# Kernel tuning notes

Hardware: AMD Instinct MI355X
Metric: run time of the kernel (lower is better)

The kernel has to match this reference:

```python
import jax, jax.numpy as jnp
import numpy as np

NQ, BS, NP_, D = 100, 8, 17, 256
NH, L, P = 8, 4, 4
DH = D // NH
DFF = 1024
SHAPES = [(92, 92), (46, 46), (23, 23), (12, 12)]
LEN_IN = sum(h * w for h, w in SHAPES)


def setup_inputs() -> dict:
    key = jax.random.key(0)
    ks = jax.random.split(key, 20)
    def nrm(k, shape, s=0.02):
        return jax.random.normal(k, shape, jnp.float32) * s
    return {
        "tgt_pose": jax.random.normal(ks[0], (NQ, BS, NP_, D), jnp.float32),
        "tgt_pose_query_pos": jax.random.normal(ks[1], (NQ, BS, NP_, D), jnp.float32),
        "tgt_pose_reference_points": jax.random.uniform(ks[2], (NQ, BS, NP_, L, 2), jnp.float32),
        "memory": jax.random.normal(ks[3], (BS, LEN_IN, D), jnp.float32),
        "w_in_w": nrm(ks[4], (3 * D, D)), "b_in_w": jnp.zeros((3 * D,), jnp.float32),
        "w_out_w": nrm(ks[5], (D, D)), "b_out_w": jnp.zeros((D,), jnp.float32),
        "w_in_a": nrm(ks[6], (3 * D, D)), "b_in_a": jnp.zeros((3 * D,), jnp.float32),
        "w_out_a": nrm(ks[7], (D, D)), "b_out_a": jnp.zeros((D,), jnp.float32),
        "w_off": nrm(ks[8], (NH * L * P * 2, D)), "b_off": nrm(ks[9], (NH * L * P * 2,), 0.1),
        "w_aw": nrm(ks[10], (NH * L * P, D)), "b_aw": jnp.zeros((NH * L * P,), jnp.float32),
        "w_val": nrm(ks[11], (D, D)), "b_val": jnp.zeros((D,), jnp.float32),
        "w_oc": nrm(ks[12], (D, D)), "b_oc": jnp.zeros((D,), jnp.float32),
        "g_w": jnp.ones((D,), jnp.float32), "be_w": jnp.zeros((D,), jnp.float32),
        "g_a": jnp.ones((D,), jnp.float32), "be_a": jnp.zeros((D,), jnp.float32),
        "g1": jnp.ones((D,), jnp.float32), "be1": jnp.zeros((D,), jnp.float32),
        "g2": jnp.ones((D,), jnp.float32), "be2": jnp.zeros((D,), jnp.float32),
        "w1": nrm(ks[13], (DFF, D)), "b1": jnp.zeros((DFF,), jnp.float32),
        "w2": nrm(ks[14], (D, DFF)), "b2": jnp.zeros((D,), jnp.float32),
        "memory_key_padding_mask": jnp.zeros((BS, LEN_IN), jnp.bool_),
        "memory_spatial_shapes": jnp.array(SHAPES, jnp.int32),
        "memory_level_start_index": jnp.array(np.cumsum([0] + [h * w for h, w in SHAPES[:-1]]), jnp.int32),
    }


def _ln(x, g, b, eps=1e-5):
    m = x.mean(-1, keepdims=True)
    v = ((x - m) ** 2).mean(-1, keepdims=True)
    return (x - m) * jax.lax.rsqrt(v + eps) * g + b


def _mha(q, k, v, w_in, b_in, w_out, b_out):
    # q,k,v: [B, S, D] batch-first; torch nn.MultiheadAttention math
    B, S, d = q.shape
    qp = (q @ w_in[:d].T + b_in[:d]).reshape(B, S, NH, DH)
    kp = (k @ w_in[d:2 * d].T + b_in[d:2 * d]).reshape(B, -1, NH, DH)
    vp = (v @ w_in[2 * d:].T + b_in[2 * d:]).reshape(B, -1, NH, DH)
    att = jax.nn.softmax(jnp.einsum('bqhd,bkhd->bhqk', qp, kp) / jnp.sqrt(jnp.float32(DH)), axis=-1)
    o = jnp.einsum('bhqk,bkhd->bqhd', att, vp).reshape(B, S, d)
    return o @ w_out.T + b_out


def _bilinear(v, loc, Hl, Wl):
    # v: [Hl*Wl, NH, DH]; loc: [Lq, NH, P, 2] normalized to [0,1]; grid_sample align_corners=False, zero pad
    x = loc[..., 0] * Wl - 0.5
    y = loc[..., 1] * Hl - 0.5
    x0 = jnp.floor(x); y0 = jnp.floor(y)
    wx = x - x0; wy = y - y0
    x0i = x0.astype(jnp.int32); y0i = y0.astype(jnp.int32)
    hid = jnp.arange(NH)[None, :, None]
    def tap(yi, xi, w):
        ok = (xi >= 0) & (xi < Wl) & (yi >= 0) & (yi < Hl)
        idx = jnp.clip(yi, 0, Hl - 1) * Wl + jnp.clip(xi, 0, Wl - 1)
        return jnp.where(ok[..., None], v[idx, hid], 0.0) * w[..., None]
    return (tap(y0i, x0i, (1 - wy) * (1 - wx)) + tap(y0i, x0i + 1, (1 - wy) * wx)
            + tap(y0i + 1, x0i, wy * (1 - wx)) + tap(y0i + 1, x0i + 1, wy * wx))


def _deform(query, ref, memory, mask, shapes, starts, w_off, b_off, w_aw, b_aw, w_val, b_val, w_oc, b_oc):
    # Multi-scale deformable attention (MSDeformAttn)
    bs, lq, d = query.shape
    value = memory @ w_val.T + b_val
    value = jnp.where(mask[..., None], 0.0, value).reshape(bs, -1, NH, DH)
    off = (query @ w_off.T + b_off).reshape(bs, lq, NH, L, P, 2)
    aw = jax.nn.softmax((query @ w_aw.T + b_aw).reshape(bs, lq, NH, L * P), axis=-1).reshape(bs, lq, NH, L, P)
    shp = np.asarray(shapes)
    st = np.asarray(starts)
    norm = jnp.asarray(shp[:, ::-1].copy(), jnp.float32)  # (W, H) per level
    loc = ref[:, :, None, :, None, :] + off / norm[None, None, None, :, None, :]
    out = jnp.zeros((bs, lq, NH, DH), query.dtype)
    for l in range(L):
        Hl, Wl = int(shp[l, 0]), int(shp[l, 1])
        v_l = value[:, int(st[l]):int(st[l]) + Hl * Wl]
        samp = jax.vmap(lambda vv, lo: _bilinear(vv, lo, Hl, Wl))(v_l, loc[:, :, :, l])
        out = out + jnp.einsum('bqhp,bqhpd->bqhd', aw[:, :, :, l], samp)
    return out.reshape(bs, lq, d) @ w_oc.T + b_oc


def _forward(tgt_pose, qpos, ref, memory, w_in_w, b_in_w, w_out_w, b_out_w, w_in_a, b_in_a, w_out_a, b_out_a, w_off, b_off, w_aw, b_aw, w_val, b_val, w_oc, b_oc, g_w, be_w, g_a, be_a, g1, be1, g2, be2, w1, b1, w2, b2, mask, shapes, starts):
    nq, bs, npt, d = tgt_pose.shape
    # within-group self-attn over keypoints (seq = np, batch = nq*bs)
    qk = (tgt_pose + qpos).reshape(nq * bs, npt, d)
    t2 = _mha(qk, qk, tgt_pose.reshape(nq * bs, npt, d), w_in_w, b_in_w, w_out_w, b_out_w).reshape(nq, bs, npt, d)
    x = _ln(tgt_pose + t2, g_w, be_w)
    # across-group self-attn over queries (seq = nq, batch = bs*np)
    y = x.reshape(nq, bs * npt, d).transpose(1, 0, 2)
    t2 = _mha(y, y, y, w_in_a, b_in_a, w_out_a, b_out_a).transpose(1, 0, 2).reshape(nq, bs, npt, d)
    x = _ln(x + t2, g_a, be_a)
    # multi-scale deformable cross-attn
    q = (x + qpos).transpose(1, 0, 2, 3).reshape(bs, nq * npt, d)
    r = ref.transpose(1, 0, 2, 3, 4).reshape(bs, nq * npt, L, 2)
    t2 = _deform(q, r, memory, mask, shapes, starts, w_off, b_off, w_aw, b_aw, w_val, b_val, w_oc, b_oc)
    t2 = t2.reshape(bs, nq, npt, d).transpose(1, 0, 2, 3)
    x = _ln(x + t2, g1, be1)
    # FFN
    ff = jax.nn.relu(x @ w1.T + b1) @ w2.T + b2
    return _ln(x + ff, g2, be2)


def reference(tgt_pose, tgt_pose_query_pos, tgt_pose_reference_points, memory, w_in_w, b_in_w, w_out_w, b_out_w, w_in_a, b_in_a, w_out_a, b_out_a, w_off, b_off, w_aw, b_aw, w_val, b_val, w_oc, b_oc, g_w, be_w, g_a, be_a, g1, be1, g2, be2, w1, b1, w2, b2, memory_key_padding_mask, memory_spatial_shapes, memory_level_start_index):
    return _forward(tgt_pose, tgt_pose_query_pos, tgt_pose_reference_points, memory, w_in_w, b_in_w, w_out_w, b_out_w, w_in_a, b_in_a, w_out_a, b_out_a, w_off, b_off, w_aw, b_aw, w_val, b_val, w_oc, b_oc, g_w, be_w, g_a, be_a, g1, be1, g2, be2, w1, b1, w2, b2, memory_key_padding_mask, memory_spatial_shapes, memory_level_start_index)
```

## Files before the change

kernel.cpp:

```cpp
#include <hip/hip_runtime.h>
#include <hip/hip_bf16.h>
#include <math.h>

#define NQd 100
#define BSd 8
#define NPTd 17
#define DIMd 256
#define NHd 8
#define DHd 32
#define DFFd 1024
#define NTOK (NQd*BSd*NPTd)
#define LENIN 11253
#define MTOK (BSd*LENIN)

typedef __attribute__((ext_vector_type(8))) short bf16x8;
typedef __attribute__((ext_vector_type(4))) short bf16x4s;
typedef __attribute__((ext_vector_type(4))) float f32x4;

__device__ inline short f2bs(float f) {
    __hip_bfloat16 h = __float2bfloat16(f);
    return *reinterpret_cast<short*>(&h);
}
__device__ inline float bs2f(short s) {
    return __uint_as_float(((unsigned)(unsigned short)s) << 16);
}

template<bool RELU, bool OUT_BF16, bool A_FP32>
__global__ __launch_bounds__(256)
void gemm_mfma(const void* __restrict__ Av, const __hip_bfloat16* __restrict__ W,
               const float* __restrict__ bias, void* __restrict__ Cv,
               int M, int N, int K, int ldc, int col0) {
    __shared__ __hip_bfloat16 LA[2][4][129][8];
    __shared__ __hip_bfloat16 LW[2][4][129][8];
    const int tid = threadIdx.x;
    const int lane = tid & 63, wave = tid >> 6;
    const int wr = wave >> 1, wc = wave & 1;
    const int m0 = blockIdx.y * 128, n0 = blockIdx.x * 128;
    const int l15 = lane & 15, lg = lane >> 4;

    const int srow = tid >> 2;
    const int koct = tid & 3;
    bf16x8 aReg[2], wReg[2];

    auto load_tile = [&](int k0) {
#pragma unroll
        for (int it = 0; it < 2; ++it) {
            const int row = srow + it * 64;
            const int gm = m0 + row;
            bf16x8 av = {0, 0, 0, 0, 0, 0, 0, 0};
            if (A_FP32) {
                if (gm < M) {
                    const float* ap = (const float*)Av + (size_t)gm * K + k0 + koct * 8;
                    float4 f0 = *(const float4*)ap;
                    float4 f1 = *(const float4*)(ap + 4);
                    av = (bf16x8){f2bs(f0.x), f2bs(f0.y), f2bs(f0.z), f2bs(f0.w),
                                  f2bs(f1.x), f2bs(f1.y), f2bs(f1.z), f2bs(f1.w)};
                }
            } else {
                if (gm < M)
                    av = *(const bf16x8*)((const __hip_bfloat16*)Av + (size_t)gm * K + k0 + koct * 8);
            }
            aReg[it] = av;
            wReg[it] = *(const bf16x8*)(W + (size_t)(n0 + row) * K + k0 + koct * 8);
        }
    };
    auto write_tile = [&](int buf) {
#pragma unroll
        for (int it = 0; it < 2; ++it) {
            const int row = srow + it * 64;
            *(bf16x8*)&LA[buf][koct][row][0] = aReg[it];
            *(bf16x8*)&LW[buf][koct][row][0] = wReg[it];
        }
    };

    f32x4 acc[4][4];
#pragma unroll
    for (int i = 0; i < 4; ++i)
#pragma unroll
        for (int j = 0; j < 4; ++j) acc[i][j] = (f32x4){0.f, 0.f, 0.f, 0.f};

    const int NT = K >> 5;
    load_tile(0);
    write_tile(0);
    __syncthreads();
    for (int t = 0; t < NT; ++t) {
        const int cur = t & 1;
        if (t + 1 < NT) load_tile((t + 1) * 32);
        bf16x8 af[4], bfr[4];
#pragma unroll
        for (int f = 0; f < 4; ++f) {
            af[f]  = *(const bf16x8*)&LA[cur][lg][wr * 64 + f * 16 + l15][0];
            bfr[f] = *(const bf16x8*)&LW[cur][lg][wc * 64 + f * 16 + l15][0];
        }
#pragma unroll
        for (int fm = 0; fm < 4; ++fm)
#pragma unroll
            for (int fn = 0; fn < 4; ++fn)
                acc[fm][fn] = __builtin_amdgcn_mfma_f32_16x16x32_bf16(af[fm], bfr[fn], acc[fm][fn], 0, 0, 0);
        if (t + 1 < NT) write_tile(cur ^ 1);
        __syncthreads();
    }

#pragma unroll
    for (int fm = 0; fm < 4; ++fm) {
        const int row = m0 + wr * 64 + fm * 16 + lg * 4;
#pragma unroll
        for (int fn = 0; fn < 4; ++fn) {
            const int coln = n0 + wc * 64 + fn * 16 + l15;
            const float bsv = bias[coln];
#pragma unroll
            for (int r = 0; r < 4; ++r) {
                const int gr = row + r;
                if (gr >= M) continue;
                float v = acc[fm][fn][r] + bsv;
                if (RELU) v = fmaxf(v, 0.f);
                if (OUT_BF16)
                    ((__hip_bfloat16*)Cv)[(size_t)gr * ldc + col0 + coln] = __float2bfloat16(v);
                else
                    ((float*)Cv)[(size_t)gr * ldc + col0 + coln] = v;
            }
        }
    }
}

__global__ void cvt_weights(const float* w0, const float* w1, const float* w2,
                            const float* w3, const float* w4, const float* w5,
                            const float* w6, const float* w7, const float* w8,
                            const float* w9, __hip_bfloat16* dst) {
    int idx = blockIdx.x * 256 + threadIdx.x;
    float v;
    if      (idx <  196608) v = w0[idx];
    else if (idx <  262144) v = w1[idx -  196608];
    else if (idx <  458752) v = w2[idx -  262144];
    else if (idx <  524288) v = w3[idx -  458752];
    else if (idx <  589824) v = w4[idx -  524288];
    else if (idx <  622592) v = w5[idx -  589824];
    else if (idx <  688128) v = w6[idx -  622592];
    else if (idx <  753664) v = w7[idx -  688128];
    else if (idx < 1015808) v = w8[idx -  753664];
    else                    v = w9[idx - 1015808];
    dst[idx] = __float2bfloat16(v);
}

__global__ void gather_rows_b(const float* __restrict__ src, const float* __restrict__ add,
                              __hip_bfloat16* __restrict__ dst, int mode) {
    int t = blockIdx.x, c = threadIdx.x;
    int r;
    if (mode == 0) r = t;
    else if (mode == 1) { int m = t / 100, q = t % 100; r = q * 136 + m; }
    else { int b = t / 1700, jj = t % 1700; int q = jj / 17, p = jj % 17; r = q * 136 + b * 17 + p; }
    float v = src[(size_t)r * 256 + c];
    if (add) v += add[(size_t)r * 256 + c];
    dst[(size_t)t * 256 + c] = __float2bfloat16(v);
}

__global__ void attn17(const float* __restrict__ qkv, __hip_bfloat16* __restrict__ out) {
    const int g = blockIdx.x, h = blockIdx.y;
    __shared__ float q[17][32], k[17][32], v[17][32], s[17][18];
    const int tid = threadIdx.x;
    for (int idx = tid; idx < 17 * 32; idx += 256) {
        int i = idx >> 5, d = idx & 31;
        size_t row = (size_t)(g * 17 + i) * 768 + h * 32 + d;
        q[i][d] = qkv[row];
        k[i][d] = qkv[row + 256];
        v[i][d] = qkv[row + 512];
    }
    __syncthreads();
    for (int idx = tid; idx < 17 * 17; idx += 256) {
        int i = idx / 17, j = idx % 17;
        float acc = 0.f;
#pragma unroll
        for (int d = 0; d < 32; ++d) acc += q[i][d] * k[j][d];
        s[i][j] = acc * 0.17677669529663688f;
    }
    __syncthreads();
    if (tid < 17) {
        float m = -1e30f;
        for (int j = 0; j < 17; ++j) m = fmaxf(m, s[tid][j]);
        float sum = 0.f;
        for (int j = 0; j < 17; ++j) { float e = __expf(s[tid][j] - m); s[tid][j] = e; sum += e; }
        float inv = 1.f / sum;
        for (int j = 0; j < 17; ++j) s[tid][j] *= inv;
    }
    __syncthreads();
    for (int idx = tid; idx < 17 * 32; idx += 256) {
        int i = idx >> 5, d = idx & 31;
        float acc = 0.f;
        for (int j = 0; j < 17; ++j) acc += s[i][j] * v[j][d];
        out[(size_t)(g * 17 + i) * 256 + h * 32 + d] = __float2bfloat16(acc);
    }
}

__global__ __launch_bounds__(128)
void attn100(const float* __restrict__ qkv, __hip_bfloat16* __restrict__ out) {
    const int g = blockIdx.x, h = blockIdx.y;
    __shared__ float Ks[100][32], Vs[100][32];
    const int tid = threadIdx.x;
    for (int idx = tid; idx < 800; idx += 128) {
        int j = idx >> 3, qd = (idx & 7) * 4;
        const float* base = qkv + (size_t)(g * 100 + j) * 768 + h * 32;
        *(float4*)&Ks[j][qd] = *(const float4*)(base + 256 + qd);
        *(float4*)&Vs[j][qd] = *(const float4*)(base + 512 + qd);
    }
    __syncthreads();
    if (tid >= 100) return;
    const float* qp = qkv + (size_t)(g * 100 + tid) * 768 + h * 32;
    float q[32];
#pragma unroll
    for (int d4 = 0; d4 < 32; d4 += 4) {
        float4 v = *(const float4*)(qp + d4);
        q[d4] = v.x; q[d4 + 1] = v.y; q[d4 + 2] = v.z; q[d4 + 3] = v.w;
    }
    float m = -1e30f, l = 0.f, o[32];
#pragma unroll
    for (int d = 0; d < 32; ++d) o[d] = 0.f;
    for (int j = 0; j < 100; ++j) {
        float s = 0.f;
#pragma unroll
        for (int d = 0; d < 32; ++d) s += q[d] * Ks[j][d];
        s *= 0.17677669529663688f;
        float nm = fmaxf(m, s);
        float f = __expf(m - nm), p = __expf(s - nm);
        l = l * f + p;
#pragma unroll
        for (int d = 0; d < 32; ++d) o[d] = o[d] * f + p * Vs[j][d];
        m = nm;
    }
    float inv = 1.f / l;
    __hip_bfloat16* op = out + (size_t)(g * 100 + tid) * 256 + h * 32;
#pragma unroll
    for (int d = 0; d < 32; ++d) op[d] = __float2bfloat16(o[d] * inv);
}

#define TPB 4
__global__ __launch_bounds__(256)
void deform_sample(const __hip_bfloat16* __restrict__ value, const float* __restrict__ off,
                   const float* __restrict__ aw, const float* __restrict__ ref,
                   __hip_bfloat16* __restrict__ out) {
    const int t0 = blockIdx.x * TPB;
    const int tid = threadIdx.x;
    __shared__ float raw[TPB][128];
    __shared__ float wgt[TPB][128];
    __shared__ int   cidx[TPB][128][4];
    __shared__ float cw[TPB][128][4];

    for (int idx = tid; idx < TPB * 128; idx += 256) {
        int tk = idx >> 7, i = idx & 127;
        raw[tk][i] = aw[(size_t)(t0 + tk) * 128 + i];
    }
    __syncthreads();
    if (tid < TPB * 8) {
        int tk = tid >> 3, h = tid & 7;
        float m = -1e30f;
        for (int i = 0; i < 16; ++i) m = fmaxf(m, raw[tk][h * 16 + i]);
        float sum = 0.f;
        float e[16];
        for (int i = 0; i < 16; ++i) { e[i] = __expf(raw[tk][h * 16 + i] - m); sum += e[i]; }
        float inv = 1.f / sum;
        for (int i = 0; i < 16; ++i) wgt[tk][h * 16 + i] = e[i] * inv;
    }
    __syncthreads();

    const int Hs[4] = {92, 46, 23, 12};
    const int Sts[4] = {0, 8464, 10580, 11109};
    for (int s = tid; s < TPB * 128; s += 256) {
        int tk = s >> 7, sid = s & 127;
        int t = t0 + tk;
        int b = t / 1700, jj = t % 1700;
        int q = jj / 17, p = jj % 17;
        int l = (sid >> 2) & 3;
        int HW = Hs[l];
        float HWf = (float)HW;
        const float* refp = ref + (size_t)((q * 8 + b) * 17 + p) * 8;
        float rx = refp[l * 2], ry = refp[l * 2 + 1];
        float ox = off[(size_t)t * 256 + sid * 2];
        float oy = off[(size_t)t * 256 + sid * 2 + 1];
        float x = (rx + ox / HWf) * HWf - 0.5f;
        float y = (ry + oy / HWf) * HWf - 0.5f;
        float x0f = floorf(x), y0f = floorf(y);
        float wx = x - x0f, wy = y - y0f;
        int xi = (int)x0f, yi = (int)y0f;
        float wg = wgt[tk][sid];
#pragma unroll
        for (int c = 0; c < 4; ++c) {
            int cy = c >> 1, cx = c & 1;
            int yy = yi + cy, xx = xi + cx;
            bool ok = (xx >= 0) && (xx < HW) && (yy >= 0) && (yy < HW);
            int yc = min(max(yy, 0), HW - 1);
            int xc = min(max(xx, 0), HW - 1);
            cidx[tk][sid][c] = Sts[l] + yc * HW + xc;
            float w = (cy ? wy : 1.f - wy) * (cx ? wx : 1.f - wx);
            cw[tk][sid][c] = ok ? wg * w : 0.f;
        }
    }
    __syncthreads();

    const int tk = tid >> 6, lane = tid & 63;
    const int h = lane >> 3, d4 = (lane & 7) * 4;
    const int t = t0 + tk;
    const int b = t / 1700;
    const __hip_bfloat16* vb = value + (size_t)b * LENIN * 256 + h * 32 + d4;
    float4 acc = make_float4(0.f, 0.f, 0.f, 0.f);
    for (int s16 = 0; s16 < 16; ++s16) {
        int sid = h * 16 + s16;
#pragma unroll
        for (int c = 0; c < 4; ++c) {
            int idx = cidx[tk][sid][c];
            float w = cw[tk][sid][c];
            bf16x4s v = *(const bf16x4s*)(vb + (size_t)idx * 256);
            acc.x += w * bs2f(v.x); acc.y += w * bs2f(v.y);
            acc.z += w * bs2f(v.z); acc.w += w * bs2f(v.w);
        }
    }
    __hip_bfloat16* op = out + (size_t)t * 256 + h * 32 + d4;
    op[0] = __float2bfloat16(acc.x);
    op[1] = __float2bfloat16(acc.y);
    op[2] = __float2bfloat16(acc.z);
    op[3] = __float2bfloat16(acc.w);
}

__global__ __launch_bounds__(256)
void res_ln(const float* __restrict__ res, const float* __restrict__ proj,
            const float* __restrict__ g, const float* __restrict__ be,
            float* __restrict__ out, __hip_bfloat16* __restrict__ outb, int mode) {
    const int wave = threadIdx.x >> 6, lane = threadIdx.x & 63;
    const int r = blockIdx.x * 4 + wave;
    int t;
    if (mode == 0) t = r;
    else if (mode == 1) { int q = r / 136, m = r % 136; t = m * 100 + q; }
    else { int q = r / 136, rem = r % 136; int b = rem / 17, p = rem % 17; t = b * 1700 + q * 17 + p; }
    const int c4 = lane * 4;
    float4 a = *(const float4*)&res[(size_t)r * 256 + c4];
    float4 p = *(const float4*)&proj[(size_t)t * 256 + c4];
    float v[4] = {a.x + p.x, a.y + p.y, a.z + p.z, a.w + p.w};
    float s = v[0] + v[1] + v[2] + v[3];
#pragma unroll
    for (int off = 32; off > 0; off >>= 1) s += __shfl_xor(s, off);
    float mean = s * (1.f / 256.f);
    float d[4], ss = 0.f;
#pragma unroll
    for (int i = 0; i < 4; ++i) { d[i] = v[i] - mean; ss += d[i] * d[i]; }
#pragma unroll
    for (int off = 32; off > 0; off >>= 1) ss += __shfl_xor(ss, off);
    float rs = rsqrtf(ss * (1.f / 256.f) + 1e-5f);
    float4 gv = *(const float4*)&g[c4];
    float4 bv = *(const float4*)&be[c4];
    float o0 = d[0] * rs * gv.x + bv.x;
    float o1 = d[1] * rs * gv.y + bv.y;
    float o2 = d[2] * rs * gv.z + bv.z;
    float o3 = d[3] * rs * gv.w + bv.w;
    *(float4*)&out[(size_t)r * 256 + c4] = make_float4(o0, o1, o2, o3);
    if (outb) {
        bf16x4s ob = {f2bs(o0), f2bs(o1), f2bs(o2), f2bs(o3)};
        *(bf16x4s*)&outb[(size_t)r * 256 + c4] = ob;
    }
}

extern "C" void kernel_launch(void* const* d_in, const int* in_sizes, int n_in,
                              void* d_out, int out_size, void* d_ws, size_t ws_size,
                              hipStream_t stream) {
    const float* tgt    = (const float*)d_in[0];
    const float* qpos   = (const float*)d_in[1];
    const float* ref    = (const float*)d_in[2];
    const float* memory = (const float*)d_in[3];
    const float* w_in_w = (const float*)d_in[4];
    const float* b_in_w = (const float*)d_in[5];
    const float* w_out_w= (const float*)d_in[6];
    const float* b_out_w= (const float*)d_in[7];
    const float* w_in_a = (const float*)d_in[8];
    const float* b_in_a = (const float*)d_in[9];
    const float* w_out_a= (const float*)d_in[10];
    const float* b_out_a= (const float*)d_in[11];
    const float* w_off  = (const float*)d_in[12];
    const float* b_off  = (const float*)d_in[13];
    const float* w_aw   = (const float*)d_in[14];
    const float* b_aw   = (const float*)d_in[15];
    const float* w_val  = (const float*)d_in[16];
    const float* b_val  = (const float*)d_in[17];
    const float* w_oc   = (const float*)d_in[18];
    const float* b_oc   = (const float*)d_in[19];
    const float* g_w    = (const float*)d_in[20];
    const float* be_w   = (const float*)d_in[21];
    const float* g_a    = (const float*)d_in[22];
    const float* be_a   = (const float*)d_in[23];
    const float* g1     = (const float*)d_in[24];
    const float* be1    = (const float*)d_in[25];
    const float* g2     = (const float*)d_in[26];
    const float* be2    = (const float*)d_in[27];
    const float* w1     = (const float*)d_in[28];
    const float* b1     = (const float*)d_in[29];
    const float* w2     = (const float*)d_in[30];
    const float* b2     = (const float*)d_in[31];

    float* X  = (float*)d_out;
    float* ws = (float*)d_ws;
    float* R1 = ws;
    float* R2 = R1 + (size_t)MTOK * 256;
    float* R3 = R2 + (size_t)NTOK * 256;
    float* R6 = R3 + (size_t)NTOK * 128;
    float* QBF= R6 + (size_t)NTOK * 128;
    float* WBF= QBF+ (size_t)NTOK * 128;

    __hip_bfloat16* R3b = (__hip_bfloat16*)R3;
    __hip_bfloat16* Qb  = (__hip_bfloat16*)QBF;
    __hip_bfloat16* Wb  = (__hip_bfloat16*)WBF;
    __hip_bfloat16* Hb  = (__hip_bfloat16*)R1;
    __hip_bfloat16* Vb  = (__hip_bfloat16*)R1;

    __hip_bfloat16* w_in_w_b  = Wb;
    __hip_bfloat16* w_out_w_b = Wb +  196608;
    __hip_bfloat16* w_in_a_b  = Wb +  262144;
    __hip_bfloat16* w_out_a_b = Wb +  458752;
    __hip_bfloat16* w_off_b   = Wb +  524288;
    __hip_bfloat16* w_aw_b    = Wb +  589824;
    __hip_bfloat16* w_val_b   = Wb +  622592;
    __hip_bfloat16* w_oc_b    = Wb +  688128;
    __hip_bfloat16* w1_b      = Wb +  753664;
    __hip_bfloat16* w2_b      = Wb + 1015808;

    cvt_weights<<<4992, 256, 0, stream>>>(w_in_w, w_out_w, w_in_a, w_out_a, w_off,
                                          w_aw, w_val, w_oc, w1, w2, Wb);

    auto gemm = [&](const __hip_bfloat16* A, const __hip_bfloat16* W, const float* b,
                    float* C, int M, int N, int K, int ldc, int col0) {
        dim3 grid(N / 128, (M + 127) / 128);
        gemm_mfma<false, false, false><<<grid, 256, 0, stream>>>(A, W, b, C, M, N, K, ldc, col0);
    };
    auto gemm_a32 = [&](const float* A, const __hip_bfloat16* W, const float* b,
                        float* C, int M, int N, int K, int ldc, int col0) {
        dim3 grid(N / 128, (M + 127) / 128);
        gemm_mfma<false, false, true><<<grid, 256, 0, stream>>>(A, W, b, C, M, N, K, ldc, col0);
    };

    gather_rows_b<<<NTOK, 256, 0, stream>>>(tgt, qpos, Qb, 0);
    gemm(Qb, w_in_w_b, b_in_w, R1, NTOK, 512, 256, 768, 0);
    gemm_a32(tgt, w_in_w_b + 512 * 256, b_in_w + 512, R1, NTOK, 256, 256, 768, 512);
    attn17<<<dim3(800, 8), 256, 0, stream>>>(R1, R3b);
    gemm((const __hip_bfloat16*)R3b, w_out_w_b, b_out_w, R2, NTOK, 256, 256, 256, 0);
    res_ln<<<NTOK / 4, 256, 0, stream>>>(tgt, R2, g_w, be_w, X, nullptr, 0);

    gather_rows_b<<<NTOK, 256, 0, stream>>>(X, nullptr, Qb, 1);
    gemm(Qb, w_in_a_b, b_in_a, R1, NTOK, 768, 256, 768, 0);
    attn100<<<dim3(136, 8), 128, 0, stream>>>(R1, R3b);
    gemm((const __hip_bfloat16*)R3b, w_out_a_b, b_out_a, R2, NTOK, 256, 256, 256, 0);
    res_ln<<<NTOK / 4, 256, 0, stream>>>(X, R2, g_a, be_a, X, nullptr, 1);

    {
        dim3 grid(256 / 128, (MTOK + 127) / 128);
        gemm_mfma<false, true, true><<<grid, 256, 0, stream>>>(memory, w_val_b, b_val, Vb,
                                                               MTOK, 256, 256, 256, 0);
    }
    gather_rows_b<<<NTOK, 256, 0, stream>>>(X, qpos, Qb, 2);
    gemm(Qb, w_off_b, b_off, R2, NTOK, 256, 256, 256, 0);
    gemm(Qb, w_aw_b, b_aw, R6, NTOK, 128, 256, 128, 0);
    deform_sample<<<NTOK / TPB, 256, 0, stream>>>(Vb, R2, R6, ref, R3b);
    gemm((const __hip_bfloat16*)R3b, w_oc_b, b_oc, R2, NTOK, 256, 256, 256, 0);
    res_ln<<<NTOK / 4, 256, 0, stream>>>(X, R2, g1, be1, X, Qb, 2);

    {
        dim3 grid(DFFd / 128, (NTOK + 127) / 128);
        gemm_mfma<true, true, false><<<grid, 256, 0, stream>>>(Qb, w1_b, b1, Hb,
                                                               NTOK, DFFd, 256, DFFd, 0);
    }
    gemm((const __hip_bfloat16*)Hb, w2_b, b2, R2, NTOK, 256, 1024, 256, 0);
    res_ln<<<NTOK / 4, 256, 0, stream>>>(X, R2, g2, be2, X, nullptr, 0);
}
```

Measured before the change: 391.9 us.

## Fuse input gathers into GEMM loads, emit bf16 intermediates, deepen GEMM prefetch

```diff
diff --git a/kernel.cpp b/kernel.cpp
--- a/kernel.cpp
+++ b/kernel.cpp
@@ -25,79 +25,128 @@
     return __uint_as_float(((unsigned)(unsigned short)s) << 16);
 }
 
-template<bool RELU, bool OUT_BF16, bool A_FP32>
+template<int AMODE, bool RELU, bool OUT_BF16>
 __global__ __launch_bounds__(256)
-void gemm_mfma(const void* __restrict__ Av, const __hip_bfloat16* __restrict__ W,
-               const float* __restrict__ bias, void* __restrict__ Cv,
-               int M, int N, int K, int ldc, int col0) {
-    __shared__ __hip_bfloat16 LA[2][4][129][8];
-    __shared__ __hip_bfloat16 LW[2][4][129][8];
+void gemm_mfma(const void* __restrict__ Av, const float* __restrict__ Aadd,
+               const __hip_bfloat16* __restrict__ W, const float* __restrict__ bias,
+               void* __restrict__ Cv, int M, int N, int K, int ldc, int col0,
+               int addMode) {
+    __shared__ __hip_bfloat16 LA[2][4][128][8];
+    __shared__ __hip_bfloat16 LW[2][4][128][8];
     const int tid = threadIdx.x;
     const int lane = tid & 63, wave = tid >> 6;
     const int wr = wave >> 1, wc = wave & 1;
     const int m0 = blockIdx.y * 128, n0 = blockIdx.x * 128;
     const int l15 = lane & 15, lg = lane >> 4;
-
-    const int srow = tid >> 2;
-    const int koct = tid & 3;
-    bf16x8 aReg[2], wReg[2];
-
-    auto load_tile = [&](int k0) {
-#pragma unroll
-        for (int it = 0; it < 2; ++it) {
-            const int row = srow + it * 64;
-            const int gm = m0 + row;
-            bf16x8 av = {0, 0, 0, 0, 0, 0, 0, 0};
-            if (A_FP32) {
-                if (gm < M) {
-                    const float* ap = (const float*)Av + (size_t)gm * K + k0 + koct * 8;
-                    float4 f0 = *(const float4*)ap;
-                    float4 f1 = *(const float4*)(ap + 4);
-                    av = (bf16x8){f2bs(f0.x), f2bs(f0.y), f2bs(f0.z), f2bs(f0.w),
-                                  f2bs(f1.x), f2bs(f1.y), f2bs(f1.z), f2bs(f1.w)};
-                }
-            } else {
-                if (gm < M)
-                    av = *(const bf16x8*)((const __hip_bfloat16*)Av + (size_t)gm * K + k0 + koct * 8);
-            }
-            aReg[it] = av;
-            wReg[it] = *(const bf16x8*)(W + (size_t)(n0 + row) * K + k0 + koct * 8);
+    const int srow = tid >> 2, koct = tid & 3;
+
+    const int gmA = m0 + srow, gmB = m0 + srow + 64;
+    const bool ok0 = gmA < M, ok1 = gmB < M;
+    int src0 = gmA, src1 = gmB;
+    if (AMODE == 3) {
+        src0 = (gmA % 100) * 136 + gmA / 100;
+        src1 = (gmB % 100) * 136 + gmB / 100;
+    }
+    const __hip_bfloat16* pAb0 = nullptr; const __hip_bfloat16* pAb1 = nullptr;
+    const float* pAf0 = nullptr; const float* pAf1 = nullptr;
+    const float* pD0 = nullptr;  const float* pD1 = nullptr;
+    bool doAdd = false;
+    if (AMODE == 0) {
+        pAb0 = (const __hip_bfloat16*)Av + (size_t)src0 * K + koct * 8;
+        pAb1 = (const __hip_bfloat16*)Av + (size_t)src1 * K + koct * 8;
+    } else {
+        pAf0 = (const float*)Av + (size_t)src0 * K + koct * 8;
+        pAf1 = (const float*)Av + (size_t)src1 * K + koct * 8;
+        if (AMODE == 2) {
+            doAdd = (addMode == 1) || (addMode == 2 && n0 < 512);
+            pD0 = Aadd + (size_t)src0 * K + koct * 8;
+            pD1 = Aadd + (size_t)src1 * K + koct * 8;
         }
-    };
-    auto write_tile = [&](int buf) {
-#pragma unroll
-        for (int it = 0; it < 2; ++it) {
-            const int row = srow + it * 64;
-            *(bf16x8*)&LA[buf][koct][row][0] = aReg[it];
-            *(bf16x8*)&LW[buf][koct][row][0] = wReg[it];
-        }
-    };
+    }
+    const __hip_bfloat16* pW0 = W + (size_t)(n0 + srow) * K + koct * 8;
+    const __hip_bfloat16* pW1 = W + (size_t)(n0 + srow + 64) * K + koct * 8;
+
+    bf16x8 aB0[2], aB1[2], wS0[2], wS1[2];
+    float4 aF0[2][2], aF1[2][2], dF0[2][2], dF1[2][2];
+    const f32x4 z4 = (f32x4){0.f, 0.f, 0.f, 0.f};
+
+#define LOAD_SET(S, kt) do {                                                   \
+    const int k0_ = (kt) * 32;                                                 \
+    if (AMODE == 0) {                                                          \
+        aB##S[0] = ok0 ? *(const bf16x8*)(pAb0 + k0_) : (bf16x8){0,0,0,0,0,0,0,0}; \
+        aB##S[1] = ok1 ? *(const bf16x8*)(pAb1 + k0_) : (bf16x8){0,0,0,0,0,0,0,0}; \
+    } else {                                                                   \
+        aF##S[0][0] = ok0 ? *(const float4*)(pAf0 + k0_)     : *(const float4*)&z4; \
+        aF##S[0][1] = ok0 ? *(const float4*)(pAf0 + k0_ + 4) : *(const float4*)&z4; \
+        aF##S[1][0] = ok1 ? *(const float4*)(pAf1 + k0_)     : *(const float4*)&z4; \
+        aF##S[1][1] = ok1 ? *(const float4*)(pAf1 + k0_ + 4) : *(const float4*)&z4; \
+        if (AMODE == 2 && doAdd) {                                             \
+            dF##S[0][0] = ok0 ? *(const float4*)(pD0 + k0_)     : *(const float4*)&z4; \
+            dF##S[0][1] = ok0 ? *(const float4*)(pD0 + k0_ + 4) : *(const float4*)&z4; \
+            dF##S[1][0] = ok1 ? *(const float4*)(pD1 + k0_)     : *(const float4*)&z4; \
+            dF##S[1][1] = ok1 ? *(const float4*)(pD1 + k0_ + 4) : *(const float4*)&z4; \
+        }                                                                      \
+    }                                                                          \
+    wS##S[0] = *(const bf16x8*)(pW0 + k0_);                                    \
+    wS##S[1] = *(const bf16x8*)(pW1 + k0_);                                    \
+} while (0)
+
+#define CVT_ROW(S, it) ((AMODE == 2 && doAdd) ?                                \
+    (bf16x8){f2bs(aF##S[it][0].x + dF##S[it][0].x), f2bs(aF##S[it][0].y + dF##S[it][0].y), \
+             f2bs(aF##S[it][0].z + dF##S[it][0].z), f2bs(aF##S[it][0].w + dF##S[it][0].w), \
+             f2bs(aF##S[it][1].x + dF##S[it][1].x), f2bs(aF##S[it][1].y + dF##S[it][1].y), \
+             f2bs(aF##S[it][1].z + dF##S[it][1].z), f2bs(aF##S[it][1].w + dF##S[it][1].w)} : \
+    (bf16x8){f2bs(aF##S[it][0].x), f2bs(aF##S[it][0].y), f2bs(aF##S[it][0].z), f2bs(aF##S[it][0].w), \
+             f2bs(aF##S[it][1].x), f2bs(aF##S[it][1].y), f2bs(aF##S[it][1].z), f2bs(aF##S[it][1].w)})
+
+#define WRITE_SET(S, buf) do {                                                 \
+    if (AMODE == 0) {                                                          \
+        *(bf16x8*)&LA[buf][koct][srow][0]      = aB##S[0];                     \
+        *(bf16x8*)&LA[buf][koct][srow + 64][0] = aB##S[1];                     \
+    } else {                                                                   \
+        *(bf16x8*)&LA[buf][koct][srow][0]      = CVT_ROW(S, 0);                \
+        *(bf16x8*)&LA[buf][koct][srow + 64][0] = CVT_ROW(S, 1);                \
+    }                                                                          \
+    *(bf16x8*)&LW[buf][koct][srow][0]      = wS##S[0];                         \
+    *(bf16x8*)&LW[buf][koct][srow + 64][0] = wS##S[1];                         \
+} while (0)
 
     f32x4 acc[4][4];
 #pragma unroll
     for (int i = 0; i < 4; ++i)
 #pragma unroll
-        for (int j = 0; j < 4; ++j) acc[i][j] = (f32x4){0.f, 0.f, 0.f, 0.f};
+        for (int j = 0; j < 4; ++j) acc[i][j] = z4;
+
+#define DO_TILE(buf)                                                           \
+    {                                                                          \
+        bf16x8 af[4], bfr[4];                                                  \
+        _Pragma("unroll")                                                      \
+        for (int f = 0; f < 4; ++f) {                                          \
+            af[f]  = *(const bf16x8*)&LA[buf][lg][wr * 64 + f * 16 + l15][0];  \
+            bfr[f] = *(const bf16x8*)&LW[buf][lg][wc * 64 + f * 16 + l15][0];  \
+        }                                                                      \
+        _Pragma("unroll")                                                      \
+        for (int fm = 0; fm < 4; ++fm)                                         \
+            _Pragma("unroll")                                                  \
+            for (int fn = 0; fn < 4; ++fn)                                     \
+                acc[fm][fn] = __builtin_amdgcn_mfma_f32_16x16x32_bf16(af[fm], bfr[fn], acc[fm][fn], 0, 0, 0); \
+    }
 
     const int NT = K >> 5;
-    load_tile(0);
-    write_tile(0);
-    __syncthreads();
-    for (int t = 0; t < NT; ++t) {
-        const int cur = t & 1;
-        if (t + 1 < NT) load_tile((t + 1) * 32);
-        bf16x8 af[4], bfr[4];
-#pragma unroll
-        for (int f = 0; f < 4; ++f) {
-            af[f]  = *(const bf16x8*)&LA[cur][lg][wr * 64 + f * 16 + l15][0];
-            bfr[f] = *(const bf16x8*)&LW[cur][lg][wc * 64 + f * 16 + l15][0];
-        }
-#pragma unroll
-        for (int fm = 0; fm < 4; ++fm)
-#pragma unroll
-            for (int fn = 0; fn < 4; ++fn)
-                acc[fm][fn] = __builtin_amdgcn_mfma_f32_16x16x32_bf16(af[fm], bfr[fn], acc[fm][fn], 0, 0, 0);
-        if (t + 1 < NT) write_tile(cur ^ 1);
+    LOAD_SET(0, 0);
+    WRITE_SET(0, 0);
+    LOAD_SET(1, 1);
+    LOAD_SET(0, 2);
+    __syncthreads();
+    for (int t = 0; t < NT; t += 2) {
+        if (t + 1 < NT) WRITE_SET(1, 1);
+        if (t + 3 < NT) LOAD_SET(1, t + 3);
+        DO_TILE(0);
+        __syncthreads();
+        if (t + 1 >= NT) break;
+        if (t + 2 < NT) WRITE_SET(0, 0);
+        if (t + 4 < NT) LOAD_SET(0, t + 4);
+        DO_TILE(1);
         __syncthreads();
     }
 
@@ -121,6 +170,10 @@
             }
         }
     }
+#undef LOAD_SET
+#undef CVT_ROW
+#undef WRITE_SET
+#undef DO_TILE
 }
 
 __global__ void cvt_weights(const float* w0, const float* w1, const float* w2,
@@ -143,27 +196,25 @@
 }
 
 __global__ void gather_rows_b(const float* __restrict__ src, const float* __restrict__ add,
-                              __hip_bfloat16* __restrict__ dst, int mode) {
+                              __hip_bfloat16* __restrict__ dst) {
     int t = blockIdx.x, c = threadIdx.x;
-    int r;
-    if (mode == 0) r = t;
-    else if (mode == 1) { int m = t / 100, q = t % 100; r = q * 136 + m; }
-    else { int b = t / 1700, jj = t % 1700; int q = jj / 17, p = jj % 17; r = q * 136 + b * 17 + p; }
-    float v = src[(size_t)r * 256 + c];
-    if (add) v += add[(size_t)r * 256 + c];
+    int b = t / 1700, jj = t % 1700;
+    int q = jj / 17, p = jj % 17;
+    int r = q * 136 + b * 17 + p;
+    float v = src[(size_t)r * 256 + c] + add[(size_t)r * 256 + c];
     dst[(size_t)t * 256 + c] = __float2bfloat16(v);
 }
 
-__global__ void attn17(const float* __restrict__ qkv, __hip_bfloat16* __restrict__ out) {
+__global__ void attn17(const __hip_bfloat16* __restrict__ qkv, __hip_bfloat16* __restrict__ out) {
     const int g = blockIdx.x, h = blockIdx.y;
     __shared__ float q[17][32], k[17][32], v[17][32], s[17][18];
     const int tid = threadIdx.x;
     for (int idx = tid; idx < 17 * 32; idx += 256) {
         int i = idx >> 5, d = idx & 31;
         size_t row = (size_t)(g * 17 + i) * 768 + h * 32 + d;
-        q[i][d] = qkv[row];
-        k[i][d] = qkv[row + 256];
-        v[i][d] = qkv[row + 512];
+        q[i][d] = bs2f(*(const short*)&qkv[row]);
+        k[i][d] = bs2f(*(const short*)&qkv[row + 256]);
+        v[i][d] = bs2f(*(const short*)&qkv[row + 512]);
     }
     __syncthreads();
     for (int idx = tid; idx < 17 * 17; idx += 256) {
@@ -192,24 +243,26 @@
 }
 
 __global__ __launch_bounds__(128)
-void attn100(const float* __restrict__ qkv, __hip_bfloat16* __restrict__ out) {
+void attn100(const __hip_bfloat16* __restrict__ qkv, __hip_bfloat16* __restrict__ out) {
     const int g = blockIdx.x, h = blockIdx.y;
     __shared__ float Ks[100][32], Vs[100][32];
     const int tid = threadIdx.x;
     for (int idx = tid; idx < 800; idx += 128) {
         int j = idx >> 3, qd = (idx & 7) * 4;
-        const float* base = qkv + (size_t)(g * 100 + j) * 768 + h * 32;
-        *(float4*)&Ks[j][qd] = *(const float4*)(base + 256 + qd);
-        *(float4*)&Vs[j][qd] = *(const float4*)(base + 512 + qd);
+        const __hip_bfloat16* base = qkv + (size_t)(g * 100 + j) * 768 + h * 32;
+        bf16x4s kv = *(const bf16x4s*)(base + 256 + qd);
+        bf16x4s vv = *(const bf16x4s*)(base + 512 + qd);
+        Ks[j][qd] = bs2f(kv.x); Ks[j][qd+1] = bs2f(kv.y); Ks[j][qd+2] = bs2f(kv.z); Ks[j][qd+3] = bs2f(kv.w);
+        Vs[j][qd] = bs2f(vv.x); Vs[j][qd+1] = bs2f(vv.y); Vs[j][qd+2] = bs2f(vv.z); Vs[j][qd+3] = bs2f(vv.w);
     }
     __syncthreads();
     if (tid >= 100) return;
-    const float* qp = qkv + (size_t)(g * 100 + tid) * 768 + h * 32;
+    const __hip_bfloat16* qp = qkv + (size_t)(g * 100 + tid) * 768 + h * 32;
     float q[32];
 #pragma unroll
     for (int d4 = 0; d4 < 32; d4 += 4) {
-        float4 v = *(const float4*)(qp + d4);
-        q[d4] = v.x; q[d4 + 1] = v.y; q[d4 + 2] = v.z; q[d4 + 3] = v.w;
+        bf16x4s v = *(const bf16x4s*)(qp + d4);
+        q[d4] = bs2f(v.x); q[d4 + 1] = bs2f(v.y); q[d4 + 2] = bs2f(v.z); q[d4 + 3] = bs2f(v.w);
     }
     float m = -1e30f, l = 0.f, o[32];
 #pragma unroll
@@ -320,7 +373,7 @@
 }
 
 __global__ __launch_bounds__(256)
-void res_ln(const float* __restrict__ res, const float* __restrict__ proj,
+void res_ln(const float* __restrict__ res, const __hip_bfloat16* __restrict__ proj,
             const float* __restrict__ g, const float* __restrict__ be,
             float* __restrict__ out, __hip_bfloat16* __restrict__ outb, int mode) {
     const int wave = threadIdx.x >> 6, lane = threadIdx.x & 63;
@@ -331,8 +384,8 @@
     else { int q = r / 136, rem = r % 136; int b = rem / 17, p = rem % 17; t = b * 1700 + q * 17 + p; }
     const int c4 = lane * 4;
     float4 a = *(const float4*)&res[(size_t)r * 256 + c4];
-    float4 p = *(const float4*)&proj[(size_t)t * 256 + c4];
-    float v[4] = {a.x + p.x, a.y + p.y, a.z + p.z, a.w + p.w};
+    bf16x4s pb = *(const bf16x4s*)&proj[(size_t)t * 256 + c4];
+    float v[4] = {a.x + bs2f(pb.x), a.y + bs2f(pb.y), a.z + bs2f(pb.z), a.w + bs2f(pb.w)};
     float s = v[0] + v[1] + v[2] + v[3];
 #pragma unroll
     for (int off = 32; off > 0; off >>= 1) s += __shfl_xor(s, off);
@@ -401,6 +454,8 @@
     float* QBF= R6 + (size_t)NTOK * 128;
     float* WBF= QBF+ (size_t)NTOK * 128;
 
+    __hip_bfloat16* R1b = (__hip_bfloat16*)R1;
+    __hip_bfloat16* R2b = (__hip_bfloat16*)R2;
     __hip_bfloat16* R3b = (__hip_bfloat16*)R3;
     __hip_bfloat16* Qb  = (__hip_bfloat16*)QBF;
     __hip_bfloat16* Wb  = (__hip_bfloat16*)WBF;
@@ -421,47 +476,37 @@
     cvt_weights<<<4992, 256, 0, stream>>>(w_in_w, w_out_w, w_in_a, w_out_a, w_off,
                                           w_aw, w_val, w_oc, w1, w2, Wb);
 
-    auto gemm = [&](const __hip_bfloat16* A, const __hip_bfloat16* W, const float* b,
-                    float* C, int M, int N, int K, int ldc, int col0) {
-        dim3 grid(N / 128, (M + 127) / 128);
-        gemm_mfma<false, false, false><<<grid, 256, 0, stream>>>(A, W, b, C, M, N, K, ldc, col0);
-    };
-    auto gemm_a32 = [&](const float* A, const __hip_bfloat16* W, const float* b,
-                        float* C, int M, int N, int K, int ldc, int col0) {
-        dim3 grid(N / 128, (M + 127) / 128);
-        gemm_mfma<false, false, true><<<grid, 256, 0, stream>>>(A, W, b, C, M, N, K, ldc, col0);
-    };
-
-    gather_rows_b<<<NTOK, 256, 0, stream>>>(tgt, qpos, Qb, 0);
-    gemm(Qb, w_in_w_b, b_in_w, R1, NTOK, 512, 256, 768, 0);
-    gemm_a32(tgt, w_in_w_b + 512 * 256, b_in_w + 512, R1, NTOK, 256, 256, 768, 512);
-    attn17<<<dim3(800, 8), 256, 0, stream>>>(R1, R3b);
-    gemm((const __hip_bfloat16*)R3b, w_out_w_b, b_out_w, R2, NTOK, 256, 256, 256, 0);
-    res_ln<<<NTOK / 4, 256, 0, stream>>>(tgt, R2, g_w, be_w, X, nullptr, 0);
-
-    gather_rows_b<<<NTOK, 256, 0, stream>>>(X, nullptr, Qb, 1);
-    gemm(Qb, w_in_a_b, b_in_a, R1, NTOK, 768, 256, 768, 0);
-    attn100<<<dim3(136, 8), 128, 0, stream>>>(R1, R3b);
-    gemm((const __hip_bfloat16*)R3b, w_out_a_b, b_out_a, R2, NTOK, 256, 256, 256, 0);
-    res_ln<<<NTOK / 4, 256, 0, stream>>>(X, R2, g_a, be_a, X, nullptr, 1);
-
-    {
-        dim3 grid(256 / 128, (MTOK + 127) / 128);
-        gemm_mfma<false, true, true><<<grid, 256, 0, stream>>>(memory, w_val_b, b_val, Vb,
-                                                               MTOK, 256, 256, 256, 0);
-    }
-    gather_rows_b<<<NTOK, 256, 0, stream>>>(X, qpos, Qb, 2);
-    gemm(Qb, w_off_b, b_off, R2, NTOK, 256, 256, 256, 0);
-    gemm(Qb, w_aw_b, b_aw, R6, NTOK, 128, 256, 128, 0);
+    const int MY = (NTOK + 127) / 128;
+
+    gemm_mfma<2, false, true><<<dim3(6, MY), 256, 0, stream>>>(
+        tgt, qpos, w_in_w_b, b_in_w, R1b, NTOK, 768, 256, 768, 0, 2);
+    attn17<<<dim3(800, 8), 256, 0, stream>>>(R1b, R3b);
+    gemm_mfma<0, false, true><<<dim3(2, MY), 256, 0, stream>>>(
+        R3b, nullptr, w_out_w_b, b_out_w, R2b, NTOK, 256, 256, 256, 0, 0);
+    res_ln<<<NTOK / 4, 256, 0, stream>>>(tgt, R2b, g_w, be_w, X, nullptr, 0);
+
+    gemm_mfma<3, false, true><<<dim3(6, MY), 256, 0, stream>>>(
+        X, nullptr, w_in_a_b, b_in_a, R1b, NTOK, 768, 256, 768, 0, 0);
+    attn100<<<dim3(136, 8), 128, 0, stream>>>(R1b, R3b);
+    gemm_mfma<0, false, true><<<dim3(2, MY), 256, 0, stream>>>(
+        R3b, nullptr, w_out_a_b, b_out_a, R2b, NTOK, 256, 256, 256, 0, 0);
+    res_ln<<<NTOK / 4, 256, 0, stream>>>(X, R2b, g_a, be_a, X, nullptr, 1);
+
+    gemm_mfma<1, false, true><<<dim3(2, (MTOK + 127) / 128), 256, 0, stream>>>(
+        memory, nullptr, w_val_b, b_val, Vb, MTOK, 256, 256, 256, 0, 0);
+    gather_rows_b<<<NTOK, 256, 0, stream>>>(X, qpos, Qb);
+    gemm_mfma<0, false, false><<<dim3(2, MY), 256, 0, stream>>>(
+        Qb, nullptr, w_off_b, b_off, R2, NTOK, 256, 256, 256, 0, 0);
+    gemm_mfma<0, false, false><<<dim3(1, MY), 256, 0, stream>>>(
+        Qb, nullptr, w_aw_b, b_aw, R6, NTOK, 128, 256, 128, 0, 0);
     deform_sample<<<NTOK / TPB, 256, 0, stream>>>(Vb, R2, R6, ref, R3b);
-    gemm((const __hip_bfloat16*)R3b, w_oc_b, b_oc, R2, NTOK, 256, 256, 256, 0);
-    res_ln<<<NTOK / 4, 256, 0, stream>>>(X, R2, g1, be1, X, Qb, 2);
-
-    {
-        dim3 grid(DFFd / 128, (NTOK + 127) / 128);
-        gemm_mfma<true, true, false><<<grid, 256, 0, stream>>>(Qb, w1_b, b1, Hb,
-                                                               NTOK, DFFd, 256, DFFd, 0);
-    }
-    gemm((const __hip_bfloat16*)Hb, w2_b, b2, R2, NTOK, 256, 1024, 256, 0);
-    res_ln<<<NTOK / 4, 256, 0, stream>>>(X, R2, g2, be2, X, nullptr, 0);
-}
+    gemm_mfma<0, false, true><<<dim3(2, MY), 256, 0, stream>>>(
+        R3b, nullptr, w_oc_b, b_oc, R2b, NTOK, 256, 256, 256, 0, 0);
+    res_ln<<<NTOK / 4, 256, 0, stream>>>(X, R2b, g1, be1, X, Qb, 2);
+
+    gemm_mfma<0, true, true><<<dim3(8, MY), 256, 0, stream>>>(
+        Qb, nullptr, w1_b, b1, Hb, NTOK, 1024, 256, 1024, 0, 0);
+    gemm_mfma<0, false, true><<<dim3(2, MY), 256, 0, stream>>>(
+        Hb, nullptr, w2_b, b2, R2b, NTOK, 256, 1024, 256, 0, 0);
+    res_ln<<<NTOK / 4, 256, 0, stream>>>(X, R2b, g2, be2, X, nullptr, 0);
+}
```

Result: slower. 623.4 us (+59.1%).

## Add 64x64-tile MFMA GEMM for narrow-N projections to raise block count

Applied to the files above, without the earlier changes.

```diff
diff --git a/kernel.cpp b/kernel.cpp
--- a/kernel.cpp
+++ b/kernel.cpp
@@ -37,9 +37,7 @@
     const int wr = wave >> 1, wc = wave & 1;
     const int m0 = blockIdx.y * 128, n0 = blockIdx.x * 128;
     const int l15 = lane & 15, lg = lane >> 4;
-
-    const int srow = tid >> 2;
-    const int koct = tid & 3;
+    const int srow = tid >> 2, koct = tid & 3;
     bf16x8 aReg[2], wReg[2];
 
     auto load_tile = [&](int k0) {
@@ -118,6 +116,92 @@
                     ((__hip_bfloat16*)Cv)[(size_t)gr * ldc + col0 + coln] = __float2bfloat16(v);
                 else
                     ((float*)Cv)[(size_t)gr * ldc + col0 + coln] = v;
+            }
+        }
+    }
+}
+
+template<bool A_FP32>
+__global__ __launch_bounds__(256)
+void gemm64(const void* __restrict__ Av, const __hip_bfloat16* __restrict__ W,
+            const float* __restrict__ bias, float* __restrict__ Cv,
+            int M, int K, int ldc, int col0) {
+    __shared__ __hip_bfloat16 LA[2][4][65][8];
+    __shared__ __hip_bfloat16 LW[2][4][65][8];
+    const int tid = threadIdx.x;
+    const int lane = tid & 63, wave = tid >> 6;
+    const int wr = wave >> 1, wc = wave & 1;
+    const int m0 = blockIdx.y * 64, n0 = blockIdx.x * 64;
+    const int l15 = lane & 15, lg = lane >> 4;
+    const int srow = tid >> 2, koct = tid & 3;
+    const int gm = m0 + srow;
+    const bool okA = gm < M;
+    const __hip_bfloat16* pAb = (const __hip_bfloat16*)Av + (size_t)(okA ? gm : 0) * K + koct * 8;
+    const float* pAf = (const float*)Av + (size_t)(okA ? gm : 0) * K + koct * 8;
+    const __hip_bfloat16* pW = W + (size_t)(n0 + srow) * K + koct * 8;
+
+    bf16x8 aR, wR;
+    float4 f0R, f1R;
+    auto load_tile = [&](int k0) {
+        if (A_FP32) {
+            f0R = okA ? *(const float4*)(pAf + k0)     : make_float4(0.f, 0.f, 0.f, 0.f);
+            f1R = okA ? *(const float4*)(pAf + k0 + 4) : make_float4(0.f, 0.f, 0.f, 0.f);
+        } else {
+            aR = okA ? *(const bf16x8*)(pAb + k0) : (bf16x8){0, 0, 0, 0, 0, 0, 0, 0};
+        }
+        wR = *(const bf16x8*)(pW + k0);
+    };
+    auto write_tile = [&](int buf) {
+        bf16x8 v;
+        if (A_FP32)
+            v = (bf16x8){f2bs(f0R.x), f2bs(f0R.y), f2bs(f0R.z), f2bs(f0R.w),
+                         f2bs(f1R.x), f2bs(f1R.y), f2bs(f1R.z), f2bs(f1R.w)};
+        else
+            v = aR;
+        *(bf16x8*)&LA[buf][koct][srow][0] = v;
+        *(bf16x8*)&LW[buf][koct][srow][0] = wR;
+    };
+
+    f32x4 acc[2][2];
+#pragma unroll
+    for (int i = 0; i < 2; ++i)
+#pragma unroll
+        for (int j = 0; j < 2; ++j) acc[i][j] = (f32x4){0.f, 0.f, 0.f, 0.f};
+
+    const int NT = K >> 5;
+    load_tile(0);
+    write_tile(0);
+    __syncthreads();
+    for (int t = 0; t < NT; ++t) {
+        const int cur = t & 1;
+        if (t + 1 < NT) load_tile((t + 1) * 32);
+        bf16x8 af[2], bfr[2];
+#pragma unroll
+        for (int f = 0; f < 2; ++f) {
+            af[f]  = *(const bf16x8*)&LA[cur][lg][wr * 32 + f * 16 + l15][0];
+            bfr[f] = *(const bf16x8*)&LW[cur][lg][wc * 32 + f * 16 + l15][0];
+        }
+#pragma unroll
+        for (int fm = 0; fm < 2; ++fm)
+#pragma unroll
+            for (int fn = 0; fn < 2; ++fn)
+                acc[fm][fn] = __builtin_amdgcn_mfma_f32_16x16x32_bf16(af[fm], bfr[fn], acc[fm][fn], 0, 0, 0);
+        if (t + 1 < NT) write_tile(cur ^ 1);
+        __syncthreads();
+    }
+
+#pragma unroll
+    for (int fm = 0; fm < 2; ++fm) {
+        const int row = m0 + wr * 32 + fm * 16 + lg * 4;
+#pragma unroll
+        for (int fn = 0; fn < 2; ++fn) {
+            const int coln = n0 + wc * 32 + fn * 16 + l15;
+            const float bsv = bias[coln];
+#pragma unroll
+            for (int r = 0; r < 4; ++r) {
+                const int gr = row + r;
+                if (gr >= M) continue;
+                Cv[(size_t)gr * ldc + col0 + coln] = acc[fm][fn][r] + bsv;
             }
         }
     }
@@ -421,47 +505,41 @@
     cvt_weights<<<4992, 256, 0, stream>>>(w_in_w, w_out_w, w_in_a, w_out_a, w_off,
                                           w_aw, w_val, w_oc, w1, w2, Wb);
 
-    auto gemm = [&](const __hip_bfloat16* A, const __hip_bfloat16* W, const float* b,
-                    float* C, int M, int N, int K, int ldc, int col0) {
-        dim3 grid(N / 128, (M + 127) / 128);
-        gemm_mfma<false, false, false><<<grid, 256, 0, stream>>>(A, W, b, C, M, N, K, ldc, col0);
-    };
-    auto gemm_a32 = [&](const float* A, const __hip_bfloat16* W, const float* b,
-                        float* C, int M, int N, int K, int ldc, int col0) {
-        dim3 grid(N / 128, (M + 127) / 128);
-        gemm_mfma<false, false, true><<<grid, 256, 0, stream>>>(A, W, b, C, M, N, K, ldc, col0);
-    };
+    const int MY64 = (NTOK + 63) / 64;
 
     gather_rows_b<<<NTOK, 256, 0, stream>>>(tgt, qpos, Qb, 0);
-    gemm(Qb, w_in_w_b, b_in_w, R1, NTOK, 512, 256, 768, 0);
-    gemm_a32(tgt, w_in_w_b + 512 * 256, b_in_w + 512, R1, NTOK, 256, 256, 768, 512);
+    gemm_mfma<false, false, false><<<dim3(4, (NTOK + 127) / 128), 256, 0, stream>>>(
+        Qb, w_in_w_b, b_in_w, R1, NTOK, 512, 256, 768, 0);
+    gemm64<true><<<dim3(4, MY64), 256, 0, stream>>>(
+        tgt, w_in_w_b + 512 * 256, b_in_w + 512, R1, NTOK, 256, 768, 512);
     attn17<<<dim3(800, 8), 256, 0, stream>>>(R1, R3b);
-    gemm((const __hip_bfloat16*)R3b, w_out_w_b, b_out_w, R2, NTOK, 256, 256, 256, 0);
+    gemm64<false><<<dim3(4, MY64), 256, 0, stream>>>(
+        R3b, w_out_w_b, b_out_w, R2, NTOK, 256, 256, 0);
     res_ln<<<NTOK / 4, 256, 0, stream>>>(tgt, R2, g_w, be_w, X, nullptr, 0);
 
     gather_rows_b<<<NTOK, 256, 0, stream>>>(X, nullptr, Qb, 1);
-    gemm(Qb, w_in_a_b, b_in_a, R1, NTOK, 768, 256, 768, 0);
+    gemm_mfma<false, false, false><<<dim3(6, (NTOK + 127) / 128), 256, 0, stream>>>(
+        Qb, w_in_a_b, b_in_a, R1, NTOK, 768, 256, 768, 0);
     attn100<<<dim3(136, 8), 128, 0, stream>>>(R1, R3b);
-    gemm((const __hip_bfloat16*)R3b, w_out_a_b, b_out_a, R2, NTOK, 256, 256, 256, 0);
+    gemm64<false><<<dim3(4, MY64), 256, 0, stream>>>(
+        R3b, w_out_a_b, b_out_a, R2, NTOK, 256, 256, 0);
     res_ln<<<NTOK / 4, 256, 0, stream>>>(X, R2, g_a, be_a, X, nullptr, 1);
 
-    {
-        dim3 grid(256 / 128, (MTOK + 127) / 128);
-        gemm_mfma<false, true, true><<<grid, 256, 0, stream>>>(memory, w_val_b, b_val, Vb,
-                                                               MTOK, 256, 256, 256, 0);
-    }
+    gemm_mfma<false, true, true><<<dim3(2, (MTOK + 127) / 128), 256, 0, stream>>>(
+        memory, w_val_b, b_val, Vb, MTOK, 256, 256, 256, 0);
     gather_rows_b<<<NTOK, 256, 0, stream>>>(X, qpos, Qb, 2);
-    gemm(Qb, w_off_b, b_off, R2, NTOK, 256, 256, 256, 0);
-    gemm(Qb, w_aw_b, b_aw, R6, NTOK, 128, 256, 128, 0);
+    gemm64<false><<<dim3(4, MY64), 256, 0, stream>>>(
+        Qb, w_off_b, b_off, R2, NTOK, 256, 256, 0);
+    gemm64<false><<<dim3(2, MY64), 256, 0, stream>>>(
+        Qb, w_aw_b, b_aw, R6, NTOK, 256, 128, 0);
     deform_sample<<<NTOK / TPB, 256, 0, stream>>>(Vb, R2, R6, ref, R3b);
-    gemm((const __hip_bfloat16*)R3b, w_oc_b, b_oc, R2, NTOK, 256, 256, 256, 0);
+    gemm64<false><<<dim3(4, MY64), 256, 0, stream>>>(
+        R3b, w_oc_b, b_oc, R2, NTOK, 256, 256, 0);
     res_ln<<<NTOK / 4, 256, 0, stream>>>(X, R2, g1, be1, X, Qb, 2);
 
-    {
-        dim3 grid(DFFd / 128, (NTOK + 127) / 128);
-        gemm_mfma<true, true, false><<<grid, 256, 0, stream>>>(Qb, w1_b, b1, Hb,
-                                                               NTOK, DFFd, 256, DFFd, 0);
-    }
-    gemm((const __hip_bfloat16*)Hb, w2_b, b2, R2, NTOK, 256, 1024, 256, 0);
+    gemm_mfma<true, true, false><<<dim3(8, (NTOK + 127) / 128), 256, 0, stream>>>(
+        Qb, w1_b, b1, Hb, NTOK, 1024, 256, 1024, 0);
+    gemm64<false><<<dim3(4, MY64), 256, 0, stream>>>(
+        (const __hip_bfloat16*)Hb, w2_b, b2, R2, NTOK, 1024, 256, 0);
     res_ln<<<NTOK / 4, 256, 0, stream>>>(X, R2, g2, be2, X, nullptr, 0);
 }
```

New measurement: 375.9 us. 4.1% less time.
